# Performance work log

Hardware: AMD Instinct MI355X
Metric: run time of the kernel (lower is better)

Reference implementation:

```python
import jax, jax.numpy as jnp
import numpy as np

B, N, C, H = 2, 2048, 512, 8
D = C // H  # head dim = 64
SCALE = C ** -0.5  # module uses heads_channels**-0.5 (full inner dim, not per-head)


def setup_inputs() -> dict:
    key = jax.random.key(0)
    ks = jax.random.split(key, 9)
    return {
        "q": jax.random.normal(ks[0], (B, N, C), jnp.float32),
        "kv": jax.random.normal(ks[1], (B, N, C), jnp.float32),
        "pos_q": jax.random.normal(ks[2], (B, N, D), jnp.float32),
        "pos_k": jax.random.normal(ks[3], (B, N, D), jnp.float32),
        "Wq": jax.random.normal(ks[4], (C, C), jnp.float32) * (C ** -0.5),
        "Wk": jax.random.normal(ks[5], (C, C), jnp.float32) * (C ** -0.5),
        "Wv": jax.random.normal(ks[6], (C, C), jnp.float32) * (C ** -0.5),
        "Wo": jax.random.normal(ks[7], (C, C), jnp.float32) * (C ** -0.5),
        "bo": jnp.zeros((C,), jnp.float32),
    }


def reference(q, kv, pos_q, pos_k, Wq, Wk, Wv, Wo, bo):
    # projections: [b n c] @ [c c] -> [b n c]
    qp = q @ Wq
    kp = kv @ Wk
    vp = kv @ Wv
    # split heads: b n (h d) -> b h n d
    split = lambda t: t.reshape(B, N, H, D).transpose(0, 2, 1, 3)
    qh, kh, vh = split(qp), split(kp), split(vp)
    # additive positional bias, broadcast over heads: b n d -> b 1 n d
    qh = qh + pos_q[:, None, :, :]
    kh = kh + pos_k[:, None, :, :]
    sim = jnp.einsum("bhid,bhjd->bhij", qh, kh) * SCALE
    attn = jax.nn.softmax(sim, axis=-1)
    out = jnp.einsum("bhij,bhjd->bhid", attn, vh)
    # merge heads: b h n d -> b n (h d)
    out = out.transpose(0, 2, 1, 3).reshape(B, N, C)
    return out @ Wo + bo
```

## Files before the change

kernel.cpp:

```cpp
#include <hip/hip_runtime.h>
#include <hip/hip_bf16.h>
#include <stdint.h>
#include <math.h>

static constexpr int kB = 2, kN = 2048, kC = 512, kH = 8, kD = 64;
static constexpr float kScaleL2E =
    (float)(0.044194173824159216 * 1.4426950408889634);
static constexpr float kShift = 12.0f;

typedef short bf16x8 __attribute__((ext_vector_type(8)));
typedef short bf16x4 __attribute__((ext_vector_type(4)));
typedef float f32x4  __attribute__((ext_vector_type(4)));

__device__ __forceinline__ float bf2f(unsigned short u) {
  union { unsigned int i; float f; } v; v.i = ((unsigned int)u) << 16; return v.f;
}
__device__ __forceinline__ unsigned short f2bf(float f) {
  union { float f; unsigned int i; } v; v.f = f;
  unsigned int x = v.i;
  return (unsigned short)((x + 0x7FFFu + ((x >> 16) & 1u)) >> 16);
}
__device__ __forceinline__ short f2bs(float f) { return (short)f2bf(f); }
__device__ __forceinline__ unsigned int pack2_t(float lo, float hi) {
  union { float f; unsigned int i; } a, b; a.f = lo; b.f = hi;
  return (b.i & 0xFFFF0000u) | (a.i >> 16);
}

__global__ __launch_bounds__(256) void prep_kernel(
    const float* __restrict__ q, const float* __restrict__ kv,
    const float* __restrict__ Wq, const float* __restrict__ Wk,
    const float* __restrict__ Wv,
    unsigned short* __restrict__ qbf, unsigned short* __restrict__ kvbf,
    unsigned short* __restrict__ wT)
{
  const int t = threadIdx.x;
  if (blockIdx.z == 0) {
    const int gid = blockIdx.x * 256 + t;
    #pragma unroll
    for (int it = 0; it < 8; ++it) {
      int i4 = gid + it * 65536;
      float4 a = *(const float4*)(q + (size_t)i4 * 4);
      float4 b = *(const float4*)(kv + (size_t)i4 * 4);
      bf16x4 ab = {f2bs(a.x), f2bs(a.y), f2bs(a.z), f2bs(a.w)};
      bf16x4 bb = {f2bs(b.x), f2bs(b.y), f2bs(b.z), f2bs(b.w)};
      *(bf16x4*)(qbf + (size_t)i4 * 4) = ab;
      *(bf16x4*)(kvbf + (size_t)i4 * 4) = bb;
    }
  } else {
    if (blockIdx.x >= 192) return;
    const int wsel = blockIdx.x >> 6;
    const int tile = blockIdx.x & 63;
    const int tr = tile >> 3, tc = tile & 7;
    const float* W = (wsel == 0) ? Wq : (wsel == 1 ? Wk : Wv);
    unsigned short* out = wT + (size_t)wsel * kC * kC;

    __shared__ __align__(16) float Ts[64][68];
    #pragma unroll
    for (int it = 0; it < 4; ++it) {
      int e = t + it * 256;
      int r = e >> 4, c4 = (e & 15) * 4;
      *(float4*)&Ts[r][c4] =
          *(const float4*)(W + (size_t)(tr * 64 + r) * kC + tc * 64 + c4);
    }
    __syncthreads();
    const int n = t >> 2, ks = (t & 3) * 16;
    unsigned short* orow = out + (size_t)(tc * 64 + n) * kC + tr * 64 + ks;
    #pragma unroll
    for (int c = 0; c < 4; ++c) {
      ushort4 o;
      o.x = f2bf(Ts[ks + c * 4 + 0][n]);
      o.y = f2bf(Ts[ks + c * 4 + 1][n]);
      o.z = f2bf(Ts[ks + c * 4 + 2][n]);
      o.w = f2bf(Ts[ks + c * 4 + 3][n]);
      *(ushort4*)(orow + c * 4) = o;
    }
  }
}

__global__ __launch_bounds__(256) void proj_kernel(
    const unsigned short* __restrict__ qbf,
    const unsigned short* __restrict__ kvbf,
    const unsigned short* __restrict__ wT,
    const float* __restrict__ pos_q,
    const float* __restrict__ pos_k,
    unsigned short* __restrict__ qh,
    unsigned short* __restrict__ kh,
    unsigned short* __restrict__ vhT)
{
  const bool kvmode = (blockIdx.z == 1);
  const unsigned short* A = kvmode ? kvbf : qbf;
  const unsigned short* Bt0 = wT + (kvmode ? (size_t)kC * kC : 0);
  const unsigned short* Bt1 = wT + 2 * (size_t)kC * kC;

  __shared__ __align__(16) unsigned short As[128][72];
  __shared__ __align__(16) unsigned short Bs[2][64][72];

  const int t = threadIdx.x;
  const int w = t >> 6, lane = t & 63;
  const int l15 = lane & 15, quad = lane >> 4;
  const int m0 = blockIdx.x * 128;
  const int n0 = blockIdx.y * 64;

  const int sr = t >> 3, sc = (t & 7) * 8;

  bf16x8 pa[4], pb0[2], pb1[2];
  #pragma unroll
  for (int i = 0; i < 4; ++i)
    pa[i] = *(const bf16x8*)(A + (size_t)(m0 + sr + i * 32) * kC + sc);
  #pragma unroll
  for (int i = 0; i < 2; ++i)
    pb0[i] = *(const bf16x8*)(Bt0 + (size_t)(n0 + sr + i * 32) * kC + sc);
  if (kvmode)
    #pragma unroll
    for (int i = 0; i < 2; ++i)
      pb1[i] = *(const bf16x8*)(Bt1 + (size_t)(n0 + sr + i * 32) * kC + sc);

  f32x4 acc0[2][4], acc1[2][4];
  #pragma unroll
  for (int si = 0; si < 2; ++si)
    #pragma unroll
    for (int ct = 0; ct < 4; ++ct) {
      acc0[si][ct] = (f32x4){0.f, 0.f, 0.f, 0.f};
      acc1[si][ct] = (f32x4){0.f, 0.f, 0.f, 0.f};
    }

  for (int k0 = 0; k0 < kC; k0 += 64) {
    if (k0) __syncthreads();
    #pragma unroll
    for (int i = 0; i < 4; ++i) *(bf16x8*)&As[sr + i * 32][sc] = pa[i];
    #pragma unroll
    for (int i = 0; i < 2; ++i) *(bf16x8*)&Bs[0][sr + i * 32][sc] = pb0[i];
    if (kvmode)
      #pragma unroll
      for (int i = 0; i < 2; ++i) *(bf16x8*)&Bs[1][sr + i * 32][sc] = pb1[i];
    __syncthreads();
    if (k0 + 64 < kC) {
      int kn = k0 + 64;
      #pragma unroll
      for (int i = 0; i < 4; ++i)
        pa[i] = *(const bf16x8*)(A + (size_t)(m0 + sr + i * 32) * kC + kn + sc);
      #pragma unroll
      for (int i = 0; i < 2; ++i)
        pb0[i] = *(const bf16x8*)(Bt0 + (size_t)(n0 + sr + i * 32) * kC + kn + sc);
      if (kvmode)
        #pragma unroll
        for (int i = 0; i < 2; ++i)
          pb1[i] = *(const bf16x8*)(Bt1 + (size_t)(n0 + sr + i * 32) * kC + kn + sc);
    }
    bf16x8 a0[2], a1[2];
    #pragma unroll
    for (int si = 0; si < 2; ++si) {
      a0[si] = *(const bf16x8*)&As[w * 32 + si * 16 + l15][quad * 8];
      a1[si] = *(const bf16x8*)&As[w * 32 + si * 16 + l15][32 + quad * 8];
    }
    #pragma unroll
    for (int ct = 0; ct < 4; ++ct) {
      bf16x8 b0 = *(const bf16x8*)&Bs[0][ct * 16 + l15][quad * 8];
      bf16x8 b1 = *(const bf16x8*)&Bs[0][ct * 16 + l15][32 + quad * 8];
      #pragma unroll
      for (int si = 0; si < 2; ++si) {
        acc0[si][ct] = __builtin_amdgcn_mfma_f32_16x16x32_bf16(a0[si], b0, acc0[si][ct], 0, 0, 0);
        acc0[si][ct] = __builtin_amdgcn_mfma_f32_16x16x32_bf16(a1[si], b1, acc0[si][ct], 0, 0, 0);
      }
      if (kvmode) {
        bf16x8 c0 = *(const bf16x8*)&Bs[1][ct * 16 + l15][quad * 8];
        bf16x8 c1 = *(const bf16x8*)&Bs[1][ct * 16 + l15][32 + quad * 8];
        #pragma unroll
        for (int si = 0; si < 2; ++si) {
          acc1[si][ct] = __builtin_amdgcn_mfma_f32_16x16x32_bf16(a0[si], c0, acc1[si][ct], 0, 0, 0);
          acc1[si][ct] = __builtin_amdgcn_mfma_f32_16x16x32_bf16(a1[si], c1, acc1[si][ct], 0, 0, 0);
        }
      }
    }
  }

  const int h = n0 >> 6;
  #pragma unroll
  for (int si = 0; si < 2; ++si)
    #pragma unroll
    for (int r = 0; r < 4; ++r) {
      int m = m0 + w * 32 + si * 16 + quad * 4 + r;
      int b = m >> 11, n_seq = m & (kN - 1);
      #pragma unroll
      for (int ct = 0; ct < 4; ++ct) {
        int d = ct * 16 + l15;
        if (!kvmode) {
          float val = (acc0[si][ct][r] +
                       pos_q[((size_t)b * kN + n_seq) * kD + d]) * kScaleL2E;
          qh[(((size_t)b * kH + h) * kN + n_seq) * kD + d] = f2bf(val);
        } else {
          float vk = acc0[si][ct][r] + pos_k[((size_t)b * kN + n_seq) * kD + d];
          kh[(((size_t)b * kH + h) * kN + n_seq) * kD + d] = f2bf(vk);
          vhT[(((size_t)b * kH + h) * kD + d) * kN + n_seq] = f2bf(acc1[si][ct][r]);
        }
      }
    }
}

__global__ __launch_bounds__(256, 2) void attn_kernel(
    const unsigned short* __restrict__ qh,
    const unsigned short* __restrict__ kh,
    const unsigned short* __restrict__ vhT,
    unsigned short* __restrict__ o0,
    unsigned short* __restrict__ o1,
    float* __restrict__ lbuf)
{
  const int bh = blockIdx.y;
  const int b = bh >> 3, h = bh & 7;
  const int q0 = blockIdx.x * 128;
  const int s = blockIdx.z;
  const int kbase = s * 1024;
  const int t = threadIdx.x;
  const int w = t >> 6, lane = t & 63;
  const int l15 = lane & 15, quad = lane >> 4;

  __shared__ __align__(16) unsigned short Kbf[2][64][72];
  __shared__ __align__(16) unsigned short Vt[2][64][72];

  const unsigned short* Qb = qh  + (size_t)bh * kN * kD;
  const unsigned short* Kb = kh  + (size_t)bh * kN * kD;
  const unsigned short* Vb = vhT + (size_t)bh * kD * kN;

  bf16x8 aq[2][2];
  #pragma unroll
  for (int g = 0; g < 2; ++g) {
    const unsigned short* qrow = Qb + (size_t)(q0 + w * 32 + g * 16 + l15) * kD;
    aq[g][0] = *(const bf16x8*)(qrow + quad * 8);
    aq[g][1] = *(const bf16x8*)(qrow + 32 + quad * 8);
  }

  const int sr = t >> 3, sc = (t & 7) * 8, sr2 = sr + 32;

  bf16x8 pk0 = *(const bf16x8*)(Kb + (size_t)(kbase + sr) * kD + sc);
  bf16x8 pk1 = *(const bf16x8*)(Kb + (size_t)(kbase + sr2) * kD + sc);
  bf16x8 pv0 = *(const bf16x8*)(Vb + (size_t)sr * kN + kbase + sc);
  bf16x8 pv1 = *(const bf16x8*)(Vb + (size_t)sr2 * kN + kbase + sc);
  *(bf16x8*)&Kbf[0][sr][sc]  = pk0;
  *(bf16x8*)&Kbf[0][sr2][sc] = pk1;
  *(bf16x8*)&Vt[0][sr][sc]   = pv0;
  *(bf16x8*)&Vt[0][sr2][sc]  = pv1;
  {
    int kt1 = kbase + 64;
    pk0 = *(const bf16x8*)(Kb + (size_t)(kt1 + sr) * kD + sc);
    pk1 = *(const bf16x8*)(Kb + (size_t)(kt1 + sr2) * kD + sc);
    pv0 = *(const bf16x8*)(Vb + (size_t)sr * kN + kt1 + sc);
    pv1 = *(const bf16x8*)(Vb + (size_t)sr2 * kN + kt1 + sc);
  }

  f32x4 o[2][4];
  #pragma unroll
  for (int g = 0; g < 2; ++g)
    #pragma unroll
    for (int nt = 0; nt < 4; ++nt) o[g][nt] = (f32x4){0.f, 0.f, 0.f, 0.f};
  float l_run[2] = {0.f, 0.f};

  const int src_a = l15 + 32 * (quad & 1);
  const int src_b = src_a + 16;
  const bool hi_sel = (quad & 2) != 0;

  for (int i = 0; i < 16; ++i) {
    __syncthreads();
    if (i + 1 < 16) {
      unsigned short (*Kw)[72] = Kbf[(i + 1) & 1];
      unsigned short (*Vw)[72] = Vt[(i + 1) & 1];
      *(bf16x8*)&Kw[sr][sc]  = pk0;
      *(bf16x8*)&Kw[sr2][sc] = pk1;
      *(bf16x8*)&Vw[sr][sc]  = pv0;
      *(bf16x8*)&Vw[sr2][sc] = pv1;
      if (i + 2 < 16) {
        int ktn = kbase + (i + 2) * 64;
        pk0 = *(const bf16x8*)(Kb + (size_t)(ktn + sr) * kD + sc);
        pk1 = *(const bf16x8*)(Kb + (size_t)(ktn + sr2) * kD + sc);
        pv0 = *(const bf16x8*)(Vb + (size_t)sr * kN + ktn + sc);
        pv1 = *(const bf16x8*)(Vb + (size_t)sr2 * kN + ktn + sc);
      }
    }
    const unsigned short (*Kr)[72] = Kbf[i & 1];
    const unsigned short (*Vr)[72] = Vt[i & 1];

    f32x4 sacc[2][4];
    #pragma unroll
    for (int ct = 0; ct < 4; ++ct) {
      bf16x8 ak0 = *(const bf16x8*)&Kr[ct * 16 + l15][quad * 8];
      bf16x8 ak1 = *(const bf16x8*)&Kr[ct * 16 + l15][32 + quad * 8];
      #pragma unroll
      for (int g = 0; g < 2; ++g) {
        f32x4 zz = (f32x4){0.f, 0.f, 0.f, 0.f};
        zz = __builtin_amdgcn_mfma_f32_16x16x32_bf16(ak0, aq[g][0], zz, 0, 0, 0);
        zz = __builtin_amdgcn_mfma_f32_16x16x32_bf16(ak1, aq[g][1], zz, 0, 0, 0);
        sacc[g][ct] = zz;
      }
    }

    union PF { unsigned int u[4]; bf16x8 v; } pf[2][2];
    #pragma unroll
    for (int g = 0; g < 2; ++g) {
      float psum = 0.f;
      #pragma unroll
      for (int ct = 0; ct < 4; ++ct)
        #pragma unroll
        for (int r = 0; r < 4; ++r) {
          float p = exp2f(sacc[g][ct][r] - kShift);
          sacc[g][ct][r] = p;
          psum += p;
        }
      psum += __shfl_xor(psum, 16);
      psum += __shfl_xor(psum, 32);
      l_run[g] += psum;

      unsigned int pk01[4], pk23[4];
      #pragma unroll
      for (int ct = 0; ct < 4; ++ct) {
        pk01[ct] = pack2_t(sacc[g][ct][0], sacc[g][ct][1]);
        pk23[ct] = pack2_t(sacc[g][ct][2], sacc[g][ct][3]);
      }
      unsigned int s01a[4], s23a[4], s01b[4], s23b[4];
      #pragma unroll
      for (int ct = 0; ct < 4; ++ct) {
        s01a[ct] = (unsigned int)__shfl((int)pk01[ct], src_a);
        s23a[ct] = (unsigned int)__shfl((int)pk23[ct], src_a);
        s01b[ct] = (unsigned int)__shfl((int)pk01[ct], src_b);
        s23b[ct] = (unsigned int)__shfl((int)pk23[ct], src_b);
      }
      pf[g][0].u[0] = hi_sel ? s01a[1] : s01a[0];
      pf[g][0].u[1] = hi_sel ? s23a[1] : s23a[0];
      pf[g][0].u[2] = hi_sel ? s01b[1] : s01b[0];
      pf[g][0].u[3] = hi_sel ? s23b[1] : s23b[0];
      pf[g][1].u[0] = hi_sel ? s01a[3] : s01a[2];
      pf[g][1].u[1] = hi_sel ? s23a[3] : s23a[2];
      pf[g][1].u[2] = hi_sel ? s01b[3] : s01b[2];
      pf[g][1].u[3] = hi_sel ? s23b[3] : s23b[2];
    }

    #pragma unroll
    for (int nt = 0; nt < 4; ++nt) {
      bf16x8 av0 = *(const bf16x8*)&Vr[nt * 16 + l15][quad * 8];
      bf16x8 av1 = *(const bf16x8*)&Vr[nt * 16 + l15][32 + quad * 8];
      #pragma unroll
      for (int g = 0; g < 2; ++g) {
        o[g][nt] = __builtin_amdgcn_mfma_f32_16x16x32_bf16(av0, pf[g][0].v, o[g][nt], 0, 0, 0);
        o[g][nt] = __builtin_amdgcn_mfma_f32_16x16x32_bf16(av1, pf[g][1].v, o[g][nt], 0, 0, 0);
      }
    }
  }

  unsigned short* od = s ? o1 : o0;
  #pragma unroll
  for (int g = 0; g < 2; ++g) {
    const int n = q0 + w * 32 + g * 16 + l15;
    unsigned short* obase = od + ((size_t)b * kN + n) * kC + h * kD + quad * 4;
    #pragma unroll
    for (int nt = 0; nt < 4; ++nt) {
      ushort4 st;
      st.x = f2bf(o[g][nt][0]);
      st.y = f2bf(o[g][nt][1]);
      st.z = f2bf(o[g][nt][2]);
      st.w = f2bf(o[g][nt][3]);
      *(ushort4*)(obase + nt * 16) = st;
    }
    if (quad == 0) lbuf[(size_t)(s * 16 + bh) * kN + n] = l_run[g];
  }
}

__global__ __launch_bounds__(256) void combine_kernel(
    unsigned short* __restrict__ o0,
    const unsigned short* __restrict__ o1,
    const float* __restrict__ lbuf)
{
  const size_t f = ((size_t)blockIdx.x * 256 + threadIdx.x) * 8;
  const int c = (int)(f & (kC - 1));
  const int n = (int)((f >> 9) & (kN - 1));
  const int b = (int)(f >> 20);
  const int bh = b * 8 + (c >> 6);
  float l0 = lbuf[(size_t)bh * kN + n];
  float l1 = lbuf[(size_t)(16 + bh) * kN + n];
  float wgt = 1.f / (l0 + l1);
  bf16x8 x = *(bf16x8*)(o0 + f);
  bf16x8 y = *(const bf16x8*)(o1 + f);
  bf16x8 r;
  #pragma unroll
  for (int j = 0; j < 8; ++j) {
    float v = (bf2f((unsigned short)x[j]) + bf2f((unsigned short)y[j])) * wgt;
    r[j] = (short)f2bf(v);
  }
  *(bf16x8*)(o0 + f) = r;
}

__global__ __launch_bounds__(256) void proj_out_kernel(
    const unsigned short* __restrict__ ao,
    const float* __restrict__ Wo,
    const float* __restrict__ bo,
    float* __restrict__ out)
{
  __shared__ __align__(16) unsigned short Wt[64][72];

  const int t = threadIdx.x;
  const int w = t >> 6, lane = t & 63;
  const int l15 = lane & 15, quad = lane >> 4;
  const int m0 = blockIdx.x * 64;
  const int n0 = blockIdx.y * 64;

  const unsigned short* arow = ao + (size_t)(m0 + w * 16 + l15) * kC;

  ushort4 pw[4];
  #pragma unroll
  for (int i = 0; i < 4; ++i) {
    int e = t + i * 256;
    int r = e >> 4, c4 = (e & 15) * 4;
    float4 wv = *(const float4*)(Wo + (size_t)r * kC + n0 + c4);
    pw[i] = make_ushort4(f2bf(wv.x), f2bf(wv.y), f2bf(wv.z), f2bf(wv.w));
  }
  bf16x8 pa0 = *(const bf16x8*)(arow + quad * 8);
  bf16x8 pa1 = *(const bf16x8*)(arow + 32 + quad * 8);

  f32x4 acc[4];
  #pragma unroll
  for (int ct = 0; ct < 4; ++ct) acc[ct] = (f32x4){0.f, 0.f, 0.f, 0.f};

  for (int k0 = 0; k0 < kC; k0 += 64) {
    if (k0) __syncthreads();
    #pragma unroll
    for (int i = 0; i < 4; ++i) {
      int e = t + i * 256;
      int r = e >> 4, c4 = (e & 15) * 4;
      Wt[c4 + 0][r] = pw[i].x;
      Wt[c4 + 1][r] = pw[i].y;
      Wt[c4 + 2][r] = pw[i].z;
      Wt[c4 + 3][r] = pw[i].w;
    }
    __syncthreads();
    bf16x8 a0 = pa0, a1 = pa1;
    if (k0 + 64 < kC) {
      int kn = k0 + 64;
      #pragma unroll
      for (int i = 0; i < 4; ++i) {
        int e = t + i * 256;
        int r = e >> 4, c4 = (e & 15) * 4;
        float4 wv = *(const float4*)(Wo + (size_t)(kn + r) * kC + n0 + c4);
        pw[i] = make_ushort4(f2bf(wv.x), f2bf(wv.y), f2bf(wv.z), f2bf(wv.w));
      }
      pa0 = *(const bf16x8*)(arow + kn + quad * 8);
      pa1 = *(const bf16x8*)(arow + kn + 32 + quad * 8);
    }
    #pragma unroll
    for (int ct = 0; ct < 4; ++ct) {
      bf16x8 b0 = *(const bf16x8*)&Wt[ct * 16 + l15][quad * 8];
      bf16x8 b1 = *(const bf16x8*)&Wt[ct * 16 + l15][32 + quad * 8];
      acc[ct] = __builtin_amdgcn_mfma_f32_16x16x32_bf16(a0, b0, acc[ct], 0, 0, 0);
      acc[ct] = __builtin_amdgcn_mfma_f32_16x16x32_bf16(a1, b1, acc[ct], 0, 0, 0);
    }
  }

  #pragma unroll
  for (int ct = 0; ct < 4; ++ct) {
    int n = n0 + ct * 16 + l15;
    float bb = bo[n];
    #pragma unroll
    for (int r = 0; r < 4; ++r) {
      int m = m0 + w * 16 + quad * 4 + r;
      out[(size_t)m * kC + n] = acc[ct][r] + bb;
    }
  }
}

extern "C" void kernel_launch(void* const* d_in, const int* in_sizes, int n_in,
                              void* d_out, int out_size, void* d_ws, size_t ws_size,
                              hipStream_t stream) {
  (void)in_sizes; (void)n_in; (void)out_size; (void)ws_size;
  const float* q     = (const float*)d_in[0];
  const float* kv    = (const float*)d_in[1];
  const float* pos_q = (const float*)d_in[2];
  const float* pos_k = (const float*)d_in[3];
  const float* Wq    = (const float*)d_in[4];
  const float* Wk    = (const float*)d_in[5];
  const float* Wv    = (const float*)d_in[6];
  const float* Wo    = (const float*)d_in[7];
  const float* bo    = (const float*)d_in[8];
  float* out = (float*)d_out;

  const size_t seg = (size_t)kB * kH * kN * kD;

  unsigned short* qbf = (unsigned short*)d_ws;
  unsigned short* qhp = qbf + seg;
  unsigned short* khp = qhp + seg;
  unsigned short* vtp = khp + seg;
  unsigned short* o0p = qbf;
  unsigned short* aop = qbf;

  unsigned short* kvbf = (unsigned short*)d_out;
  unsigned short* wT   = kvbf + seg;
  unsigned short* o1p  = kvbf;
  float*          lbp  = (float*)(kvbf + seg);

  dim3 blk(256);
  prep_kernel<<<dim3(256, 1, 2), blk, 0, stream>>>(q, kv, Wq, Wk, Wv, qbf, kvbf, wT);
  proj_kernel<<<dim3(32, 8, 2), blk, 0, stream>>>(qbf, kvbf, wT, pos_q, pos_k,
                                                  qhp, khp, vtp);
  attn_kernel<<<dim3(16, 16, 2), blk, 0, stream>>>(qhp, khp, vtp, o0p, o1p, lbp);
  combine_kernel<<<dim3(1024), blk, 0, stream>>>(o0p, o1p, lbp);
  proj_out_kernel<<<dim3(64, 8), blk, 0, stream>>>(aop, Wo, bo, out);
}
```

Before: 167.2 us.

## Split attention keys four ways, load K/V directly from global, combine fp32 partials

The attention kernel now splits the key range into four chunks instead of two, doubling the grid to 1024 blocks. It drops the LDS double-buffered K/V staging and __syncthreads, and each wave reads its MFMA operands straight from global memory through the caches. Partial outputs are stored in fp32 in a dedicated workspace and summed by a wider combine kernel. The aim is more occupancy and parallelism without barrier stalls, at the cost of redundant global/L2 traffic across waves, larger fp32 partial buffers, and more workspace use.

```diff
diff --git a/kernel.cpp b/kernel.cpp
--- a/kernel.cpp
+++ b/kernel.cpp
@@ -7,6 +7,8 @@
 static constexpr float kScaleL2E =
     (float)(0.044194173824159216 * 1.4426950408889634);
 static constexpr float kShift = 12.0f;
+static constexpr int kSplit = 4;
+static constexpr size_t kSegF = (size_t)kB * kN * kC;
 
 typedef short bf16x8 __attribute__((ext_vector_type(8)));
 typedef short bf16x4 __attribute__((ext_vector_type(4)));
@@ -197,25 +199,21 @@
     }
 }
 
-__global__ __launch_bounds__(256, 2) void attn_kernel(
+__global__ __launch_bounds__(256) void attn_kernel(
     const unsigned short* __restrict__ qh,
     const unsigned short* __restrict__ kh,
     const unsigned short* __restrict__ vhT,
-    unsigned short* __restrict__ o0,
-    unsigned short* __restrict__ o1,
+    float* __restrict__ opart,
     float* __restrict__ lbuf)
 {
   const int bh = blockIdx.y;
   const int b = bh >> 3, h = bh & 7;
   const int q0 = blockIdx.x * 128;
   const int s = blockIdx.z;
-  const int kbase = s * 1024;
+  const int kbase = s * (kN / kSplit);
   const int t = threadIdx.x;
   const int w = t >> 6, lane = t & 63;
   const int l15 = lane & 15, quad = lane >> 4;
-
-  __shared__ __align__(16) unsigned short Kbf[2][64][72];
-  __shared__ __align__(16) unsigned short Vt[2][64][72];
 
   const unsigned short* Qb = qh  + (size_t)bh * kN * kD;
   const unsigned short* Kb = kh  + (size_t)bh * kN * kD;
@@ -229,24 +227,6 @@
     aq[g][1] = *(const bf16x8*)(qrow + 32 + quad * 8);
   }
 
-  const int sr = t >> 3, sc = (t & 7) * 8, sr2 = sr + 32;
-
-  bf16x8 pk0 = *(const bf16x8*)(Kb + (size_t)(kbase + sr) * kD + sc);
-  bf16x8 pk1 = *(const bf16x8*)(Kb + (size_t)(kbase + sr2) * kD + sc);
-  bf16x8 pv0 = *(const bf16x8*)(Vb + (size_t)sr * kN + kbase + sc);
-  bf16x8 pv1 = *(const bf16x8*)(Vb + (size_t)sr2 * kN + kbase + sc);
-  *(bf16x8*)&Kbf[0][sr][sc]  = pk0;
-  *(bf16x8*)&Kbf[0][sr2][sc] = pk1;
-  *(bf16x8*)&Vt[0][sr][sc]   = pv0;
-  *(bf16x8*)&Vt[0][sr2][sc]  = pv1;
-  {
-    int kt1 = kbase + 64;
-    pk0 = *(const bf16x8*)(Kb + (size_t)(kt1 + sr) * kD + sc);
-    pk1 = *(const bf16x8*)(Kb + (size_t)(kt1 + sr2) * kD + sc);
-    pv0 = *(const bf16x8*)(Vb + (size_t)sr * kN + kt1 + sc);
-    pv1 = *(const bf16x8*)(Vb + (size_t)sr2 * kN + kt1 + sc);
-  }
-
   f32x4 o[2][4];
   #pragma unroll
   for (int g = 0; g < 2; ++g)
@@ -258,36 +238,26 @@
   const int src_b = src_a + 16;
   const bool hi_sel = (quad & 2) != 0;
 
-  for (int i = 0; i < 16; ++i) {
-    __syncthreads();
-    if (i + 1 < 16) {
-      unsigned short (*Kw)[72] = Kbf[(i + 1) & 1];
-      unsigned short (*Vw)[72] = Vt[(i + 1) & 1];
-      *(bf16x8*)&Kw[sr][sc]  = pk0;
-      *(bf16x8*)&Kw[sr2][sc] = pk1;
-      *(bf16x8*)&Vw[sr][sc]  = pv0;
-      *(bf16x8*)&Vw[sr2][sc] = pv1;
-      if (i + 2 < 16) {
-        int ktn = kbase + (i + 2) * 64;
-        pk0 = *(const bf16x8*)(Kb + (size_t)(ktn + sr) * kD + sc);
-        pk1 = *(const bf16x8*)(Kb + (size_t)(ktn + sr2) * kD + sc);
-        pv0 = *(const bf16x8*)(Vb + (size_t)sr * kN + ktn + sc);
-        pv1 = *(const bf16x8*)(Vb + (size_t)sr2 * kN + ktn + sc);
-      }
-    }
-    const unsigned short (*Kr)[72] = Kbf[i & 1];
-    const unsigned short (*Vr)[72] = Vt[i & 1];
+  for (int kt = kbase; kt < kbase + kN / kSplit; kt += 64) {
+    bf16x8 ak0[4], ak1[4], av0[4], av1[4];
+    #pragma unroll
+    for (int i = 0; i < 4; ++i) {
+      const unsigned short* kr = Kb + (size_t)(kt + i * 16 + l15) * kD + quad * 8;
+      ak0[i] = *(const bf16x8*)kr;
+      ak1[i] = *(const bf16x8*)(kr + 32);
+      const unsigned short* vr = Vb + (size_t)(i * 16 + l15) * kN + kt + quad * 8;
+      av0[i] = *(const bf16x8*)vr;
+      av1[i] = *(const bf16x8*)(vr + 32);
+    }
 
     f32x4 sacc[2][4];
     #pragma unroll
     for (int ct = 0; ct < 4; ++ct) {
-      bf16x8 ak0 = *(const bf16x8*)&Kr[ct * 16 + l15][quad * 8];
-      bf16x8 ak1 = *(const bf16x8*)&Kr[ct * 16 + l15][32 + quad * 8];
       #pragma unroll
       for (int g = 0; g < 2; ++g) {
         f32x4 zz = (f32x4){0.f, 0.f, 0.f, 0.f};
-        zz = __builtin_amdgcn_mfma_f32_16x16x32_bf16(ak0, aq[g][0], zz, 0, 0, 0);
-        zz = __builtin_amdgcn_mfma_f32_16x16x32_bf16(ak1, aq[g][1], zz, 0, 0, 0);
+        zz = __builtin_amdgcn_mfma_f32_16x16x32_bf16(ak0[ct], aq[g][0], zz, 0, 0, 0);
+        zz = __builtin_amdgcn_mfma_f32_16x16x32_bf16(ak1[ct], aq[g][1], zz, 0, 0, 0);
         sacc[g][ct] = zz;
       }
     }
@@ -334,56 +304,54 @@
 
     #pragma unroll
     for (int nt = 0; nt < 4; ++nt) {
-      bf16x8 av0 = *(const bf16x8*)&Vr[nt * 16 + l15][quad * 8];
-      bf16x8 av1 = *(const bf16x8*)&Vr[nt * 16 + l15][32 + quad * 8];
       #pragma unroll
       for (int g = 0; g < 2; ++g) {
-        o[g][nt] = __builtin_amdgcn_mfma_f32_16x16x32_bf16(av0, pf[g][0].v, o[g][nt], 0, 0, 0);
-        o[g][nt] = __builtin_amdgcn_mfma_f32_16x16x32_bf16(av1, pf[g][1].v, o[g][nt], 0, 0, 0);
-      }
-    }
-  }
-
-  unsigned short* od = s ? o1 : o0;
+        o[g][nt] = __builtin_amdgcn_mfma_f32_16x16x32_bf16(av0[nt], pf[g][0].v, o[g][nt], 0, 0, 0);
+        o[g][nt] = __builtin_amdgcn_mfma_f32_16x16x32_bf16(av1[nt], pf[g][1].v, o[g][nt], 0, 0, 0);
+      }
+    }
+  }
+
+  float* od = opart + (size_t)s * kSegF;
   #pragma unroll
   for (int g = 0; g < 2; ++g) {
     const int n = q0 + w * 32 + g * 16 + l15;
-    unsigned short* obase = od + ((size_t)b * kN + n) * kC + h * kD + quad * 4;
-    #pragma unroll
-    for (int nt = 0; nt < 4; ++nt) {
-      ushort4 st;
-      st.x = f2bf(o[g][nt][0]);
-      st.y = f2bf(o[g][nt][1]);
-      st.z = f2bf(o[g][nt][2]);
-      st.w = f2bf(o[g][nt][3]);
-      *(ushort4*)(obase + nt * 16) = st;
-    }
+    float* obase = od + ((size_t)b * kN + n) * kC + h * kD + quad * 4;
+    #pragma unroll
+    for (int nt = 0; nt < 4; ++nt)
+      *(float4*)(obase + nt * 16) =
+          make_float4(o[g][nt][0], o[g][nt][1], o[g][nt][2], o[g][nt][3]);
     if (quad == 0) lbuf[(size_t)(s * 16 + bh) * kN + n] = l_run[g];
   }
 }
 
 __global__ __launch_bounds__(256) void combine_kernel(
-    unsigned short* __restrict__ o0,
-    const unsigned short* __restrict__ o1,
-    const float* __restrict__ lbuf)
+    const float* __restrict__ opart,
+    const float* __restrict__ lbuf,
+    unsigned short* __restrict__ ao)
 {
-  const size_t f = ((size_t)blockIdx.x * 256 + threadIdx.x) * 8;
+  const size_t f = ((size_t)blockIdx.x * 256 + threadIdx.x) * 4;
   const int c = (int)(f & (kC - 1));
   const int n = (int)((f >> 9) & (kN - 1));
   const int b = (int)(f >> 20);
   const int bh = b * 8 + (c >> 6);
-  float l0 = lbuf[(size_t)bh * kN + n];
-  float l1 = lbuf[(size_t)(16 + bh) * kN + n];
-  float wgt = 1.f / (l0 + l1);
-  bf16x8 x = *(bf16x8*)(o0 + f);
-  bf16x8 y = *(const bf16x8*)(o1 + f);
-  bf16x8 r;
-  #pragma unroll
-  for (int j = 0; j < 8; ++j) {
-    float v = (bf2f((unsigned short)x[j]) + bf2f((unsigned short)y[j])) * wgt;
-    r[j] = (short)f2bf(v);
-  }
-  *(bf16x8*)(o0 + f) = r;
+  float lsum = 0.f;
+  #pragma unroll
+  for (int s = 0; s < kSplit; ++s)
+    lsum += lbuf[(size_t)(s * 16 + bh) * kN + n];
+  float wgt = 1.f / lsum;
+  float4 acc = make_float4(0.f, 0.f, 0.f, 0.f);
+  #pragma unroll
+  for (int s = 0; s < kSplit; ++s) {
+    float4 v = *(const float4*)(opart + (size_t)s * kSegF + f);
+    acc.x += v.x; acc.y += v.y; acc.z += v.z; acc.w += v.w;
+  }
+  ushort4 r;
+  r.x = f2bf(acc.x * wgt);
+  r.y = f2bf(acc.y * wgt);
+  r.z = f2bf(acc.z * wgt);
+  r.w = f2bf(acc.w * wgt);
+  *(ushort4*)(ao + f) = r;
 }
 
 __global__ __launch_bounds__(256) void proj_out_kernel(
@@ -480,23 +448,21 @@
 
   const size_t seg = (size_t)kB * kH * kN * kD;
 
-  unsigned short* qbf = (unsigned short*)d_ws;
-  unsigned short* qhp = qbf + seg;
-  unsigned short* khp = qhp + seg;
-  unsigned short* vtp = khp + seg;
-  unsigned short* o0p = qbf;
-  unsigned short* aop = qbf;
-
-  unsigned short* kvbf = (unsigned short*)d_out;
+  unsigned short* qbf  = (unsigned short*)d_ws;
+  unsigned short* kvbf = qbf + seg;
   unsigned short* wT   = kvbf + seg;
-  unsigned short* o1p  = kvbf;
-  float*          lbp  = (float*)(kvbf + seg);
+  unsigned short* qhp  = wT + 3 * (size_t)kC * kC;
+  unsigned short* khp  = qhp + seg;
+  unsigned short* vtp  = khp + seg;
+  float* opart = (float*)(vtp + seg);
+  float* lbuf  = opart + (size_t)kSplit * kSegF;
+  unsigned short* aop = (unsigned short*)(lbuf + (size_t)kSplit * 16 * kN);
 
   dim3 blk(256);
   prep_kernel<<<dim3(256, 1, 2), blk, 0, stream>>>(q, kv, Wq, Wk, Wv, qbf, kvbf, wT);
   proj_kernel<<<dim3(32, 8, 2), blk, 0, stream>>>(qbf, kvbf, wT, pos_q, pos_k,
                                                   qhp, khp, vtp);
-  attn_kernel<<<dim3(16, 16, 2), blk, 0, stream>>>(qhp, khp, vtp, o0p, o1p, lbp);
-  combine_kernel<<<dim3(1024), blk, 0, stream>>>(o0p, o1p, lbp);
+  attn_kernel<<<dim3(16, 16, kSplit), blk, 0, stream>>>(qhp, khp, vtp, opart, lbuf);
+  combine_kernel<<<dim3(2048), blk, 0, stream>>>(opart, lbuf, aop);
   proj_out_kernel<<<dim3(64, 8), blk, 0, stream>>>(aop, Wo, bo, out);
 }
```

Result: slower. 202.3 us (+21.0%).
